# Performance work log

Hardware: AMD Instinct MI355X
Metric: run time of the kernel (lower is better)

## Reference

```python
import jax, jax.numpy as jnp
import numpy as np

B, T, N_POS, N_ACT, H = 256, 512, 128, 32, 512
D = N_POS + N_ACT


def setup_inputs() -> dict:
    key = jax.random.key(0)
    ks = jax.random.split(key, 10)
    s_ih = 1.0 / np.sqrt(H)  # torch LSTMCell default uniform(-1/sqrt(H), 1/sqrt(H))
    xav_hc = np.sqrt(2.0 / (B + H))  # xavier_normal_ on [B,H] h0/c0
    return {
        "observation": jax.random.normal(ks[0], (B, T, N_POS), dtype=jnp.float32),
        "action": jax.random.normal(ks[1], (B, T, N_ACT), dtype=jnp.float32),
        "W_ih": jax.random.uniform(ks[2], (4 * H, D), jnp.float32, -s_ih, s_ih),
        "W_hh": jax.random.uniform(ks[3], (4 * H, H), jnp.float32, -s_ih, s_ih),
        "b_ih": jax.random.uniform(ks[4], (4 * H,), jnp.float32, -s_ih, s_ih),
        "b_hh": jax.random.uniform(ks[5], (4 * H,), jnp.float32, -s_ih, s_ih),
        "W_out": jax.random.uniform(ks[6], (1, H), jnp.float32, -s_ih, s_ih),
        "b_out": jax.random.uniform(ks[7], (1,), jnp.float32, -s_ih, s_ih),
        "h0": jax.random.normal(ks[8], (B, H), dtype=jnp.float32) * xav_hc,
        "c0": jax.random.normal(ks[9], (B, H), dtype=jnp.float32) * xav_hc,
    }


def reference(observation, action, W_ih, W_hh, b_ih, b_hh, W_out, b_out, h0, c0):
    # x: [B,T,D] -> scan over time [T,B,D]
    x = jnp.concatenate([observation, action], axis=-1)
    xs = jnp.transpose(x, (1, 0, 2))
    b = b_ih + b_hh

    def step(carry, x_t):
        h, c = carry
        gates = x_t @ W_ih.T + h @ W_hh.T + b  # [B, 4H]
        i, f, g, o = jnp.split(gates, 4, axis=-1)
        i = jax.nn.sigmoid(i)
        f = jax.nn.sigmoid(f)
        g = jnp.tanh(g)
        o = jax.nn.sigmoid(o)
        c_new = f * c + i * g
        h_new = o * jnp.tanh(c_new)
        y = h_new @ W_out.T + b_out  # [B, 1]
        return (h_new, c_new), y

    _, ys = jax.lax.scan(step, (h0, c0), xs)  # ys: [T, B, 1]
    return jnp.transpose(ys, (1, 0, 2))  # [B, T, 1]
```

## Files before the change

### kernel.cpp

```cpp
#include <hip/hip_runtime.h>
#include <math.h>


namespace {
constexpr int kT = 512, kH = 512;

typedef _Float16 v8h __attribute__((ext_vector_type(8)));
typedef float v4f __attribute__((ext_vector_type(4)));
typedef unsigned long long ull;
typedef ull v2u __attribute__((ext_vector_type(2)));

__device__ __forceinline__ ull ld64sc(const ull* p, bool sys) {
    return sys ? __hip_atomic_load(p, __ATOMIC_RELAXED, __HIP_MEMORY_SCOPE_SYSTEM)
               : __hip_atomic_load(p, __ATOMIC_RELAXED, __HIP_MEMORY_SCOPE_AGENT);
}
__device__ __forceinline__ unsigned ld32sc(const unsigned* p, bool sys) {
    return sys ? __hip_atomic_load(p, __ATOMIC_RELAXED, __HIP_MEMORY_SCOPE_SYSTEM)
               : __hip_atomic_load(p, __ATOMIC_RELAXED, __HIP_MEMORY_SCOPE_AGENT);
}
__device__ __forceinline__ void st32sc(unsigned* p, unsigned v, bool sys) {
    if (sys) __hip_atomic_store(p, v, __ATOMIC_RELAXED, __HIP_MEMORY_SCOPE_SYSTEM);
    else     __hip_atomic_store(p, v, __ATOMIC_RELAXED, __HIP_MEMORY_SCOPE_WORKGROUP);
}
__device__ __forceinline__ unsigned ld_sys32(const unsigned* p) {
    return __hip_atomic_load(p, __ATOMIC_RELAXED, __HIP_MEMORY_SCOPE_SYSTEM);
}

__device__ __forceinline__ float sigf(float x) {
    return __builtin_amdgcn_rcpf(1.0f + __builtin_amdgcn_exp2f(x * -1.442695041f));
}
__device__ __forceinline__ float tanhff(float x) {
    return fmaf(-2.0f,
                __builtin_amdgcn_rcpf(__builtin_amdgcn_exp2f(x * 2.885390082f) + 1.0f),
                1.0f);
}

__global__ void lstm_init(const float* __restrict__ h0, _Float16* __restrict__ hfA,
                          unsigned* __restrict__ ctrl) {
    int i = blockIdx.x * blockDim.x + threadIdx.x;
    int bb = i >> 9, j = i & 511;
    int bgrp = bb >> 4, b = bb & 15;
    int ck = j >> 5, jl = j & 31, qf = jl >> 3, e = jl & 7;
    int slot = (qf * 16 + b) ^ ck;
    hfA[bgrp * 8192 + ck * 512 + slot * 8 + e] = (_Float16)h0[i];
    if (i < 1152) ctrl[i] = 0u;
}

__global__ __launch_bounds__(256, 1) void lstm_persist(
    const float* __restrict__ obs, const float* __restrict__ act,
    const float* __restrict__ Wih, const float* __restrict__ Whh,
    const float* __restrict__ bih, const float* __restrict__ bhh,
    const float* __restrict__ Wout, const float* __restrict__ bout_p,
    const float* __restrict__ c0,
    _Float16* __restrict__ hfA, _Float16* __restrict__ hfB,
    unsigned* __restrict__ ctrl, float* __restrict__ out) {

    __shared__ __align__(16) char xbuf[2][5 * 1024];
    __shared__ __align__(16) char hbuf[2][16 * 1024];
    __shared__ float ypart[2][4];
    __shared__ float ytail[2];
    __shared__ int sh_role[3];

    const int tid = threadIdx.x;
    const int w = tid >> 6, ln = tid & 63;
    const int lm = ln & 15, q = ln >> 4;

    unsigned* flags = ctrl;
    unsigned* regcnt = ctrl + 1024;
    unsigned* regtotal = ctrl + 1032;

    if (tid == 0) {
        int x = __builtin_amdgcn_s_getreg(20 | (31 << 11)) & 7;
        unsigned slot = atomicAdd(&regcnt[x], 1u);
        asm volatile("s_waitcnt vmcnt(0)" ::: "memory");
        atomicAdd(regtotal, 1u);
        while (ld_sys32(regtotal) < 256u) __builtin_amdgcn_s_sleep(8);
        unsigned cnt[8];
#pragma unroll
        for (int i = 0; i < 8; ++i) cnt[i] = ld_sys32(&regcnt[i]);
        int pure_base = 0, total_pure = 0, lbase = 0;
        for (int i = 0; i < 8; ++i) {
            if (i < x) { pure_base += cnt[i] >> 4; lbase += cnt[i] & 15; }
            total_pure += cnt[i] >> 4;
        }
        int px16 = (int)(cnt[x] >> 4) * 16;
        int bg, jv, sv;
        if ((int)slot < px16) {
            bg = pure_base + ((int)slot >> 4); jv = slot & 15; sv = 0;
        } else {
            int lr = lbase + ((int)slot - px16);
            bg = total_pure + (lr >> 4); jv = lr & 15; sv = 1;
        }
        sh_role[0] = bg; sh_role[1] = jv; sh_role[2] = sv;
    }
    __syncthreads();
    const int bgrp = sh_role[0], jg = sh_role[1];
    const bool sysS = sh_role[2] != 0;
    const int yb = bgrp * 16 + jg;
    unsigned* myflags = flags + bgrp * 64;

    v8h afrag[2][21];
    {
        const int jj = lm >> 2, gt = lm & 3;
#pragma unroll
        for (int ti = 0; ti < 2; ++ti) {
            const int grow = gt * kH + jg * 32 + w * 8 + jj * 2 + ti;
#pragma unroll
            for (int kc = 0; kc < 21; ++kc) {
                const int k0 = kc * 32 + q * 8;
                const float* src = (k0 < 160) ? (Wih + grow * 160 + k0)
                                              : (Whh + (size_t)grow * kH + (k0 - 160));
                float4 A = *(const float4*)src;
                float4 Bv = *(const float4*)(src + 4);
                v8h f;
                f[0] = (_Float16)A.x;  f[1] = (_Float16)A.y;
                f[2] = (_Float16)A.z;  f[3] = (_Float16)A.w;
                f[4] = (_Float16)Bv.x; f[5] = (_Float16)Bv.y;
                f[6] = (_Float16)Bv.z; f[7] = (_Float16)Bv.w;
                afrag[ti][kc] = f;
            }
        }
    }
    float biasv[2][4];
    float creg[2];
#pragma unroll
    for (int ti = 0; ti < 2; ++ti) {
        const int jloc = jg * 32 + w * 8 + q * 2 + ti;
#pragma unroll
        for (int g = 0; g < 4; ++g)
            biasv[ti][g] = bih[g * kH + jloc] + bhh[g * kH + jloc];
        creg[ti] = c0[(size_t)(bgrp * 16 + lm) * kH + jloc];
    }

    const float bout0 = bout_p[0];
    const float2 wout2 = *(const float2*)(Wout + 2 * tid);
    float4 wout4 = make_float4(0.f, 0.f, 0.f, 0.f);
    if (tid < 128) wout4 = *(const float4*)(Wout + tid * 4);

    const int st = tid - 96, xb = st & 15, c10 = st >> 4;
    const bool isX = (tid >= 96);
    float4 xr[4];

    auto x_load = [&](int tt) {
        if (isX) {
            const size_t brow = (size_t)(bgrp * 16 + xb) * kT + tt;
            const float* p = (c10 < 8) ? (obs + brow * 128 + c10 * 16)
                                       : (act + brow * 32 + (c10 - 8) * 16);
            xr[0] = *(const float4*)(p);
            xr[1] = *(const float4*)(p + 4);
            xr[2] = *(const float4*)(p + 8);
            xr[3] = *(const float4*)(p + 12);
        }
    };
    auto x_write = [&](char* xbase) {
        if (isX) {
            const int kcx = c10 >> 1;
#pragma unroll
            for (int ii = 0; ii < 2; ++ii) {
                const int qx = (2 * c10 + ii) & 3;
                const int slot = (qx * 16 + xb) ^ kcx;
                float4 a = xr[2 * ii], b = xr[2 * ii + 1];
                v8h f;
                f[0] = (_Float16)a.x; f[1] = (_Float16)a.y;
                f[2] = (_Float16)a.z; f[3] = (_Float16)a.w;
                f[4] = (_Float16)b.x; f[5] = (_Float16)b.y;
                f[6] = (_Float16)b.z; f[7] = (_Float16)b.w;
                *(v8h*)(xbase + kcx * 1024 + slot * 16) = f;
            }
        }
    };

    x_load(0);
    x_write(xbuf[0]);
    x_load(1);
    __syncthreads();

    char* const hfAc = (char*)hfA;
    char* const hfBc = (char*)hfB;

#pragma unroll 1
    for (int t = 0; t < kT; ++t) {
        const char* hsrcB = ((t & 1) ? hfBc : hfAc) + (size_t)bgrp * 16384;
        char* hdstB = ((t & 1) ? hfAc : hfBc) + (size_t)bgrp * 16384;
        const char* xcur = xbuf[t & 1];
        char* hreg = hbuf[t & 1];

        if (t > 0) {
            const unsigned tgt = (unsigned)t;
            const unsigned* fp = myflags + ln;
            while (true) {
                unsigned v = ld32sc(fp, sysS);
                if (__all((int)(v >= tgt))) break;
            }
        }

        ull u[8];
#pragma unroll
        for (int k = 0; k < 4; ++k) {
            const ull* sp = (const ull*)(hsrcB + k * 4096 + tid * 16);
            u[2 * k]     = ld64sc(sp, sysS);
            u[2 * k + 1] = ld64sc(sp + 1, sysS);
        }

        v4f a0 = {biasv[0][0], biasv[0][1], biasv[0][2], biasv[0][3]};
        v4f a1 = {biasv[1][0], biasv[1][1], biasv[1][2], biasv[1][3]};
#pragma unroll
        for (int kc = 0; kc < 5; ++kc) {
            v8h bfr = *(const v8h*)(xcur + kc * 1024 + (ln ^ kc) * 16);
            a0 = __builtin_amdgcn_mfma_f32_16x16x32_f16(afrag[0][kc], bfr, a0, 0, 0, 0);
            a1 = __builtin_amdgcn_mfma_f32_16x16x32_f16(afrag[1][kc], bfr, a1, 0, 0, 0);
        }

#pragma unroll
        for (int k = 0; k < 4; ++k) {
            v2u val = {u[2 * k], u[2 * k + 1]};
            *(v2u*)(hreg + k * 4096 + tid * 16) = val;
        }
        if (t < kT - 1) x_write(xbuf[(t + 1) & 1]);
        __syncthreads();

        if (t >= 2 && tid == 64) {
            const float* yp = ypart[(t - 1) & 1];
            out[(size_t)yb * kT + (t - 2)] = bout0 + yp[0] + yp[1] + yp[2] + yp[3];
        }

        v4f b0 = {0.f, 0.f, 0.f, 0.f}, b1 = {0.f, 0.f, 0.f, 0.f};
#pragma unroll
        for (int ck = 0; ck < 8; ++ck) {
            v8h bfr = *(const v8h*)(hreg + ck * 1024 + (ln ^ ck) * 16);
            a0 = __builtin_amdgcn_mfma_f32_16x16x32_f16(afrag[0][5 + ck], bfr, a0, 0, 0, 0);
            a1 = __builtin_amdgcn_mfma_f32_16x16x32_f16(afrag[1][5 + ck], bfr, a1, 0, 0, 0);
        }
#pragma unroll
        for (int ck = 8; ck < 16; ++ck) {
            v8h bfr = *(const v8h*)(hreg + ck * 1024 + (ln ^ ck) * 16);
            b0 = __builtin_amdgcn_mfma_f32_16x16x32_f16(afrag[0][5 + ck], bfr, b0, 0, 0, 0);
            b1 = __builtin_amdgcn_mfma_f32_16x16x32_f16(afrag[1][5 + ck], bfr, b1, 0, 0, 0);
        }

        union { unsigned u32; _Float16 h2[2]; } pk;
#pragma unroll
        for (int ti = 0; ti < 2; ++ti) {
            v4f a = ti ? (a1 + b1) : (a0 + b0);
            float iv = sigf(a[0]), fv = sigf(a[1]);
            float gv = tanhff(a[2]), ov = sigf(a[3]);
            creg[ti] = fmaf(fv, creg[ti], iv * gv);
            pk.h2[ti] = (_Float16)(ov * tanhff(creg[ti]));
        }
        st32sc((unsigned*)(hdstB + jg * 1024 + (w * 16 + (lm ^ jg)) * 16 + q * 4),
               pk.u32, sysS);
        asm volatile("s_waitcnt vmcnt(0)" ::: "memory");
        if (ln == 0) st32sc(myflags + jg * 4 + w, (unsigned)(t + 1), sysS);

        if (t > 0) {
            const int k = 2 * tid;
            const int ck = k >> 5, qy = (k >> 3) & 3, e = k & 7;
            const int slot = (qy * 16 + jg) ^ ck;
            union { unsigned uu; _Float16 hh[2]; } cv;
            cv.uu = *(const unsigned*)(hreg + ck * 1024 + slot * 16 + e * 2);
            float p = (float)cv.hh[0] * wout2.x + (float)cv.hh[1] * wout2.y;
#pragma unroll
            for (int s = 32; s; s >>= 1) p += __shfl_xor(p, s);
            if (ln == 0) ypart[t & 1][w] = p;
        }

        if (t < kT - 2) x_load(t + 2);
    }

    if (tid < 64) {
        const unsigned* fp = myflags + ln;
        while (true) {
            unsigned v = ld32sc(fp, sysS);
            if (__all((int)(v >= (unsigned)kT))) break;
            __builtin_amdgcn_s_sleep(1);
        }
    }
    __syncthreads();
    if (tid == 64) {
        const float* yp = ypart[1];
        out[(size_t)yb * kT + (kT - 2)] = bout0 + yp[0] + yp[1] + yp[2] + yp[3];
    }
    if (tid < 128) {
        const int j0 = tid * 4;
        const int ck = j0 >> 5, qf = (j0 >> 3) & 3, e0 = j0 & 7;
        const int slot = (qf * 16 + jg) ^ ck;
        union { ull uu; _Float16 h4[4]; } cv;
        cv.uu = ld64sc((const ull*)(hfAc + (size_t)bgrp * 16384 + ck * 1024 +
                                    slot * 16 + e0 * 2), sysS);
        float p = (float)cv.h4[0] * wout4.x + (float)cv.h4[1] * wout4.y +
                  (float)cv.h4[2] * wout4.z + (float)cv.h4[3] * wout4.w;
#pragma unroll
        for (int s = 32; s; s >>= 1) p += __shfl_xor(p, s);
        if (ln == 0) ytail[w] = p;
    }
    __syncthreads();
    if (tid == 0) out[(size_t)yb * kT + (kT - 1)] = ytail[0] + ytail[1] + bout0;
}

}

extern "C" void kernel_launch(void* const* d_in, const int* in_sizes, int n_in,
                              void* d_out, int out_size, void* d_ws, size_t ws_size,
                              hipStream_t stream) {
    const float* obs  = (const float*)d_in[0];
    const float* act  = (const float*)d_in[1];
    const float* Wih  = (const float*)d_in[2];
    const float* Whh  = (const float*)d_in[3];
    const float* bih  = (const float*)d_in[4];
    const float* bhh  = (const float*)d_in[5];
    const float* Wout = (const float*)d_in[6];
    const float* bout = (const float*)d_in[7];
    const float* h0   = (const float*)d_in[8];
    const float* c0   = (const float*)d_in[9];
    float* out = (float*)d_out;

    char* ws = (char*)d_ws;
    _Float16* hfA = (_Float16*)ws;
    _Float16* hfB = (_Float16*)(ws + 262144);
    unsigned* ctrl = (unsigned*)(ws + 524288);

    lstm_init<<<512, 256, 0, stream>>>(h0, hfA, ctrl);
    lstm_persist<<<256, 256, 0, stream>>>(obs, act, Wih, Whh, bih, bhh, Wout, bout,
                                          c0, hfA, hfB, ctrl, out);
}
```

Measured before the change: 1.315 ms.

## Replace per-step flag barrier with step-tagged hidden-state words

Each published hidden-state pair is now stored as a 64-bit word holding the fp16 data plus the step number. Readers load those words directly and spin until every tag matches, which removes the separate flag array, the store drain wait, and the serialized flag-poll-then-load round trip. The cost is twice the exchange traffic and a re-load loop over stale groups. It also relies on each 64-bit relaxed store being observed atomically.

```diff
diff --git a/kernel.cpp b/kernel.cpp
--- a/kernel.cpp
+++ b/kernel.cpp
@@ -7,18 +7,14 @@
 
 typedef _Float16 v8h __attribute__((ext_vector_type(8)));
 typedef float v4f __attribute__((ext_vector_type(4)));
+typedef unsigned v4u __attribute__((ext_vector_type(4)));
 typedef unsigned long long ull;
-typedef ull v2u __attribute__((ext_vector_type(2)));
 
 __device__ __forceinline__ ull ld64sc(const ull* p, bool sys) {
     return sys ? __hip_atomic_load(p, __ATOMIC_RELAXED, __HIP_MEMORY_SCOPE_SYSTEM)
                : __hip_atomic_load(p, __ATOMIC_RELAXED, __HIP_MEMORY_SCOPE_AGENT);
 }
-__device__ __forceinline__ unsigned ld32sc(const unsigned* p, bool sys) {
-    return sys ? __hip_atomic_load(p, __ATOMIC_RELAXED, __HIP_MEMORY_SCOPE_SYSTEM)
-               : __hip_atomic_load(p, __ATOMIC_RELAXED, __HIP_MEMORY_SCOPE_AGENT);
-}
-__device__ __forceinline__ void st32sc(unsigned* p, unsigned v, bool sys) {
+__device__ __forceinline__ void st64sc(ull* p, ull v, bool sys) {
     if (sys) __hip_atomic_store(p, v, __ATOMIC_RELAXED, __HIP_MEMORY_SCOPE_SYSTEM);
     else     __hip_atomic_store(p, v, __ATOMIC_RELAXED, __HIP_MEMORY_SCOPE_WORKGROUP);
 }
@@ -35,15 +31,21 @@
                 1.0f);
 }
 
-__global__ void lstm_init(const float* __restrict__ h0, _Float16* __restrict__ hfA,
-                          unsigned* __restrict__ ctrl) {
+__global__ void lstm_init(const float* __restrict__ h0, ull* __restrict__ hfA,
+                          ull* __restrict__ hfB, unsigned* __restrict__ ctrl) {
     int i = blockIdx.x * blockDim.x + threadIdx.x;
-    int bb = i >> 9, j = i & 511;
+    int bb = i >> 8, pr = i & 255;
+    int j0 = pr * 2;
+    int ck = j0 >> 5, jl = j0 & 31, qf = jl >> 3, qe = (jl & 7) >> 1;
     int bgrp = bb >> 4, b = bb & 15;
-    int ck = j >> 5, jl = j & 31, qf = jl >> 3, e = jl & 7;
-    int slot = (qf * 16 + b) ^ ck;
-    hfA[bgrp * 8192 + ck * 512 + slot * 8 + e] = (_Float16)h0[i];
-    if (i < 1152) ctrl[i] = 0u;
+    int slot = qf * 16 + (b ^ ck);
+    size_t off = (size_t)bgrp * 4096 + ck * 256 + slot * 4 + qe;
+    union { unsigned u; _Float16 h[2]; } pk;
+    pk.h[0] = (_Float16)h0[(size_t)bb * kH + j0];
+    pk.h[1] = (_Float16)h0[(size_t)bb * kH + j0 + 1];
+    hfA[off] = (ull)pk.u;
+    hfB[off] = 0ull;
+    if (i < 16) ctrl[1024 + i] = 0u;
 }
 
 __global__ __launch_bounds__(256, 1) void lstm_persist(
@@ -52,7 +54,7 @@
     const float* __restrict__ bih, const float* __restrict__ bhh,
     const float* __restrict__ Wout, const float* __restrict__ bout_p,
     const float* __restrict__ c0,
-    _Float16* __restrict__ hfA, _Float16* __restrict__ hfB,
+    ull* __restrict__ hfA, ull* __restrict__ hfB,
     unsigned* __restrict__ ctrl, float* __restrict__ out) {
 
     __shared__ __align__(16) char xbuf[2][5 * 1024];
@@ -65,7 +67,6 @@
     const int w = tid >> 6, ln = tid & 63;
     const int lm = ln & 15, q = ln >> 4;
 
-    unsigned* flags = ctrl;
     unsigned* regcnt = ctrl + 1024;
     unsigned* regtotal = ctrl + 1032;
 
@@ -97,7 +98,6 @@
     const int bgrp = sh_role[0], jg = sh_role[1];
     const bool sysS = sh_role[2] != 0;
     const int yb = bgrp * 16 + jg;
-    unsigned* myflags = flags + bgrp * 64;
 
     v8h afrag[2][21];
     {
@@ -175,31 +175,22 @@
     x_load(1);
     __syncthreads();
 
-    char* const hfAc = (char*)hfA;
-    char* const hfBc = (char*)hfB;
-
 #pragma unroll 1
     for (int t = 0; t < kT; ++t) {
-        const char* hsrcB = ((t & 1) ? hfBc : hfAc) + (size_t)bgrp * 16384;
-        char* hdstB = ((t & 1) ? hfAc : hfBc) + (size_t)bgrp * 16384;
+        const ull* tsrc = ((t & 1) ? hfB : hfA) + (size_t)bgrp * 4096;
+        ull* tdst = ((t & 1) ? hfA : hfB) + (size_t)bgrp * 4096;
         const char* xcur = xbuf[t & 1];
         char* hreg = hbuf[t & 1];
-
-        if (t > 0) {
-            const unsigned tgt = (unsigned)t;
-            const unsigned* fp = myflags + ln;
-            while (true) {
-                unsigned v = ld32sc(fp, sysS);
-                if (__all((int)(v >= tgt))) break;
-            }
-        }
-
-        ull u[8];
-#pragma unroll
-        for (int k = 0; k < 4; ++k) {
-            const ull* sp = (const ull*)(hsrcB + k * 4096 + tid * 16);
-            u[2 * k]     = ld64sc(sp, sysS);
-            u[2 * k + 1] = ld64sc(sp + 1, sysS);
+        const unsigned tg = (unsigned)t;
+
+        ull eg[16];
+#pragma unroll
+        for (int g = 0; g < 4; ++g) {
+            const ull* sp = tsrc + g * 1024 + tid * 4;
+            eg[4 * g + 0] = ld64sc(sp + 0, sysS);
+            eg[4 * g + 1] = ld64sc(sp + 1, sysS);
+            eg[4 * g + 2] = ld64sc(sp + 2, sysS);
+            eg[4 * g + 3] = ld64sc(sp + 3, sysS);
         }
 
         v4f a0 = {biasv[0][0], biasv[0][1], biasv[0][2], biasv[0][3]};
@@ -211,10 +202,34 @@
             a1 = __builtin_amdgcn_mfma_f32_16x16x32_f16(afrag[1][kc], bfr, a1, 0, 0, 0);
         }
 
-#pragma unroll
-        for (int k = 0; k < 4; ++k) {
-            v2u val = {u[2 * k], u[2 * k + 1]};
-            *(v2u*)(hreg + k * 4096 + tid * 16) = val;
+        while (true) {
+            unsigned stale = 0u;
+#pragma unroll
+            for (int g = 0; g < 4; ++g) {
+                unsigned d = ((unsigned)(eg[4 * g + 0] >> 32) ^ tg) |
+                             ((unsigned)(eg[4 * g + 1] >> 32) ^ tg) |
+                             ((unsigned)(eg[4 * g + 2] >> 32) ^ tg) |
+                             ((unsigned)(eg[4 * g + 3] >> 32) ^ tg);
+                if (d) stale |= (1u << g);
+            }
+            if (__all((int)(stale == 0u))) break;
+#pragma unroll
+            for (int g = 0; g < 4; ++g) {
+                if (stale & (1u << g)) {
+                    const ull* sp = tsrc + g * 1024 + tid * 4;
+                    eg[4 * g + 0] = ld64sc(sp + 0, sysS);
+                    eg[4 * g + 1] = ld64sc(sp + 1, sysS);
+                    eg[4 * g + 2] = ld64sc(sp + 2, sysS);
+                    eg[4 * g + 3] = ld64sc(sp + 3, sysS);
+                }
+            }
+        }
+
+#pragma unroll
+        for (int g = 0; g < 4; ++g) {
+            v4u dv = {(unsigned)eg[4 * g + 0], (unsigned)eg[4 * g + 1],
+                      (unsigned)eg[4 * g + 2], (unsigned)eg[4 * g + 3]};
+            *(v4u*)(hreg + g * 4096 + tid * 16) = dv;
         }
         if (t < kT - 1) x_write(xbuf[(t + 1) & 1]);
         __syncthreads();
@@ -247,10 +262,8 @@
             creg[ti] = fmaf(fv, creg[ti], iv * gv);
             pk.h2[ti] = (_Float16)(ov * tanhff(creg[ti]));
         }
-        st32sc((unsigned*)(hdstB + jg * 1024 + (w * 16 + (lm ^ jg)) * 16 + q * 4),
-               pk.u32, sysS);
-        asm volatile("s_waitcnt vmcnt(0)" ::: "memory");
-        if (ln == 0) st32sc(myflags + jg * 4 + w, (unsigned)(t + 1), sysS);
+        st64sc(tdst + jg * 256 + (w * 16 + (lm ^ jg)) * 4 + q,
+               ((ull)(tg + 1) << 32) | (ull)pk.u32, sysS);
 
         if (t > 0) {
             const int k = 2 * tid;
@@ -267,33 +280,31 @@
         if (t < kT - 2) x_load(t + 2);
     }
 
-    if (tid < 64) {
-        const unsigned* fp = myflags + ln;
+    if (tid < 128) {
+        const int j0 = tid * 4;
+        const int ck = j0 >> 5, jl = j0 & 31, qf = jl >> 3, qe0 = (jl & 7) >> 1;
+        const ull* tp = hfA + (size_t)bgrp * 4096 + ck * 256 +
+                        (qf * 16 + (jg ^ ck)) * 4 + qe0;
+        ull u0, u1;
         while (true) {
-            unsigned v = ld32sc(fp, sysS);
-            if (__all((int)(v >= (unsigned)kT))) break;
-            __builtin_amdgcn_s_sleep(1);
-        }
+            u0 = ld64sc(tp + 0, sysS);
+            u1 = ld64sc(tp + 1, sysS);
+            unsigned d = ((unsigned)(u0 >> 32) ^ 512u) | ((unsigned)(u1 >> 32) ^ 512u);
+            if (__all((int)(d == 0u))) break;
+        }
+        union { unsigned u; _Float16 h[2]; } a0v, a1v;
+        a0v.u = (unsigned)u0; a1v.u = (unsigned)u1;
+        float p = (float)a0v.h[0] * wout4.x + (float)a0v.h[1] * wout4.y +
+                  (float)a1v.h[0] * wout4.z + (float)a1v.h[1] * wout4.w;
+#pragma unroll
+        for (int s = 32; s; s >>= 1) p += __shfl_xor(p, s);
+        if (ln == 0) ytail[w] = p;
     }
     __syncthreads();
     if (tid == 64) {
         const float* yp = ypart[1];
         out[(size_t)yb * kT + (kT - 2)] = bout0 + yp[0] + yp[1] + yp[2] + yp[3];
     }
-    if (tid < 128) {
-        const int j0 = tid * 4;
-        const int ck = j0 >> 5, qf = (j0 >> 3) & 3, e0 = j0 & 7;
-        const int slot = (qf * 16 + jg) ^ ck;
-        union { ull uu; _Float16 h4[4]; } cv;
-        cv.uu = ld64sc((const ull*)(hfAc + (size_t)bgrp * 16384 + ck * 1024 +
-                                    slot * 16 + e0 * 2), sysS);
-        float p = (float)cv.h4[0] * wout4.x + (float)cv.h4[1] * wout4.y +
-                  (float)cv.h4[2] * wout4.z + (float)cv.h4[3] * wout4.w;
-#pragma unroll
-        for (int s = 32; s; s >>= 1) p += __shfl_xor(p, s);
-        if (ln == 0) ytail[w] = p;
-    }
-    __syncthreads();
     if (tid == 0) out[(size_t)yb * kT + (kT - 1)] = ytail[0] + ytail[1] + bout0;
 }
 
@@ -315,11 +326,11 @@
     float* out = (float*)d_out;
 
     char* ws = (char*)d_ws;
-    _Float16* hfA = (_Float16*)ws;
-    _Float16* hfB = (_Float16*)(ws + 262144);
-    unsigned* ctrl = (unsigned*)(ws + 524288);
-
-    lstm_init<<<512, 256, 0, stream>>>(h0, hfA, ctrl);
+    ull* hfA = (ull*)ws;
+    ull* hfB = (ull*)(ws + 524288);
+    unsigned* ctrl = (unsigned*)(ws + 1048576);
+
+    lstm_init<<<256, 256, 0, stream>>>(h0, hfA, hfB, ctrl);
     lstm_persist<<<256, 256, 0, stream>>>(obs, act, Wih, Whh, bih, bhh, Wout, bout,
                                           c0, hfA, hfB, ctrl, out);
 }
```

After: 1.514 ms. 15.1% more time.
